# Performance work log

Measured on AMD Instinct MI355X. Metric: run time of the kernel, lower is better.

The kernel has to match this reference:

```python
import jax, jax.numpy as jnp
import numpy as np

N_EMBD = 2048
N_HEAD = 16
HEAD_DIM = N_EMBD // N_HEAD  # 128
ROPE_BASE = 10000.0


def _rope_cos_sin(T, dim, dtype):
    theta = 1.0 / (ROPE_BASE ** (jnp.arange(0, dim, 2, dtype=jnp.float32) / dim))  # [dim/2]
    freqs = jnp.arange(T, dtype=jnp.float32)[:, None] * theta[None, :]  # [T, dim/2]
    return jnp.cos(freqs).astype(dtype), jnp.sin(freqs).astype(dtype)


def _apply_rope(t, cos, sin):
    # t: [B,H,T,D]; interleaved (even, odd) pairs form complex numbers.
    B, H, T, D = t.shape
    tr = t.reshape(B, H, T, D // 2, 2)
    a, b = tr[..., 0], tr[..., 1]
    # (a + ib) * (cos + i sin)
    out = jnp.stack([a * cos - b * sin, a * sin + b * cos], axis=-1)
    return out.reshape(B, H, T, D)


def setup_inputs() -> dict:
    key = jax.random.key(0)
    k1, k2, k3 = jax.random.split(key, 3)
    B, T, C = 2, 2048, N_EMBD
    s = 1.0 / np.sqrt(C)
    return {
        "x": jax.random.normal(k1, (B, T, C), dtype=jnp.float32),
        "w_att": jax.random.normal(k2, (3 * C, C), dtype=jnp.float32) * s,
        "b_att": jnp.zeros((3 * C,), dtype=jnp.float32),
        "w_proj": jax.random.normal(k3, (C, C), dtype=jnp.float32) * s,
        "b_proj": jnp.zeros((C,), dtype=jnp.float32),
    }


def reference(x, w_att, b_att, w_proj, b_proj):
    B, T, C = x.shape
    H, D = N_HEAD, HEAD_DIM
    qkv = x @ w_att.T + b_att  # [B,T,3C]
    q, k, v = jnp.split(qkv, 3, axis=-1)
    # [B,T,C] -> [B,H,T,D]
    q, k, v = (t.reshape(B, T, H, D).transpose(0, 2, 1, 3) for t in (q, k, v))
    cos, sin = _rope_cos_sin(T, D, jnp.float32)  # [T, D/2]
    cos = cos[None, None]  # [1,1,T,D/2]
    sin = sin[None, None]
    q = _apply_rope(q, cos, sin)
    k = _apply_rope(k, cos, sin)
    # causal SDPA
    scale = 1.0 / np.sqrt(D)
    scores = jnp.einsum('bhqd,bhkd->bhqk', q, k) * scale
    mask = jnp.tril(jnp.ones((T, T), dtype=bool))
    scores = jnp.where(mask, scores, jnp.finfo(scores.dtype).min)
    attn = jax.nn.softmax(scores, axis=-1)
    y = jnp.einsum('bhqk,bhkd->bhqd', attn, v)  # [B,H,T,D]
    y = y.transpose(0, 2, 1, 3).reshape(B, T, C)
    return y @ w_proj.T + b_proj
```

## Files before the change

kernel.cpp:

```cpp
#include <hip/hip_runtime.h>
#include <hip/hip_bf16.h>
#include <math.h>

#define DEVI __device__ __forceinline__

typedef __attribute__((ext_vector_type(8))) short bf16x8;
typedef __attribute__((ext_vector_type(4))) float f32x4;

constexpr int Bn = 2;
constexpr int Tn = 2048;
constexpr int Cn = 2048;
constexpr int Hn = 16;
constexpr int Dn = 128;
constexpr int Mrows = Bn * Tn;
constexpr int Nqkv = 3 * Cn;
constexpr int BH = Bn * Hn;
constexpr int NKT = Cn / 32;

DEVI f32x4 mfma16x16(bf16x8 a, bf16x8 b, f32x4 c) {
    return __builtin_amdgcn_mfma_f32_16x16x32_bf16(a, b, c, 0, 0, 0);
}

DEVI bf16x8 load8(const __hip_bfloat16* p) {
    return *(const bf16x8*)p;
}

DEVI short bf16bits(float f) {
    union { __hip_bfloat16 b; short s; } u;
    u.b = __float2bfloat16(f);
    return u.s;
}

typedef const __attribute__((address_space(1))) void* gas1_t;
typedef __attribute__((address_space(3))) void* las3_t;
DEVI void stage16(const __hip_bfloat16* g, __hip_bfloat16* l) {
    __builtin_amdgcn_global_load_lds((gas1_t)g, (las3_t)l, 16, 0, 0);
}

DEVI bf16x8 lds8(const short* tile, int byte_off) {
    return *(const bf16x8*)((const char*)tile + byte_off);
}

__global__ __launch_bounds__(256) void cvt_kernel(
    const float* __restrict__ src, __hip_bfloat16* __restrict__ dst)
{
    const size_t i8 = ((size_t)blockIdx.x * 256 + threadIdx.x) * 8;
    const float4 a = *(const float4*)(src + i8);
    const float4 b = *(const float4*)(src + i8 + 4);
    union { bf16x8 v; __hip_bfloat16 h[8]; } u;
    u.h[0] = __float2bfloat16(a.x); u.h[1] = __float2bfloat16(a.y);
    u.h[2] = __float2bfloat16(a.z); u.h[3] = __float2bfloat16(a.w);
    u.h[4] = __float2bfloat16(b.x); u.h[5] = __float2bfloat16(b.y);
    u.h[6] = __float2bfloat16(b.z); u.h[7] = __float2bfloat16(b.w);
    *(bf16x8*)(dst + i8) = u.v;
}

__global__ __launch_bounds__(256) void qkv_gemm_kernel(
    const __hip_bfloat16* __restrict__ xb,
    const __hip_bfloat16* __restrict__ wab,
    const float* __restrict__ bias,
    __hip_bfloat16* __restrict__ Qo,
    __hip_bfloat16* __restrict__ Ko,
    __hip_bfloat16* __restrict__ Vt)
{
    __shared__ __align__(16) __hip_bfloat16 As[2][128 * 32];
    __shared__ __align__(16) __hip_bfloat16 Bs[2][128 * 32];
    const int tid  = threadIdx.x;
    const int lane = tid & 63;
    const int wid  = tid >> 6;
    const int quad = lane >> 4;
    const int l16  = lane & 15;
    const int bm = blockIdx.y * 128;
    const int bn = blockIdx.x * 128;
    const int wm = (wid >> 1) * 64;
    const int wn = (wid & 1) * 64;

    const int lr = lane >> 2;
    const int lc = (lane & 3) * 8;
    const int r0 = 32 * wid;
    const __hip_bfloat16* Ag0 = xb  + (size_t)(bm + r0 + lr) * Cn + lc;
    const __hip_bfloat16* Ag1 = xb  + (size_t)(bm + r0 + 16 + lr) * Cn + lc;
    const __hip_bfloat16* Bg0 = wab + (size_t)(bn + r0 + lr) * Cn + lc;
    const __hip_bfloat16* Bg1 = wab + (size_t)(bn + r0 + 16 + lr) * Cn + lc;
    const int lbase0 = r0 * 32 + lane * 8;
    const int lbase1 = (r0 + 16) * 32 + lane * 8;

    const f32x4 zero = {0.f, 0.f, 0.f, 0.f};
    f32x4 acc[4][4];
#pragma unroll
    for (int i = 0; i < 4; ++i)
#pragma unroll
        for (int j = 0; j < 4; ++j) acc[i][j] = zero;

    stage16(Ag0, &As[0][lbase0]);
    stage16(Ag1, &As[0][lbase1]);
    stage16(Bg0, &Bs[0][lbase0]);
    stage16(Bg1, &Bs[0][lbase1]);
    __syncthreads();

    for (int kt = 0; kt < NKT; ++kt) {
        const int cur = kt & 1;
        if (kt + 1 < NKT) {
            const int kn = (kt + 1) * 32;
            stage16(Ag0 + kn, &As[cur ^ 1][lbase0]);
            stage16(Ag1 + kn, &As[cur ^ 1][lbase1]);
            stage16(Bg0 + kn, &Bs[cur ^ 1][lbase0]);
            stage16(Bg1 + kn, &Bs[cur ^ 1][lbase1]);
        }
        bf16x8 af[4], bfr[4];
#pragma unroll
        for (int i = 0; i < 4; ++i)
            af[i] = load8(&As[cur][(wm + i * 16 + l16) * 32 + quad * 8]);
#pragma unroll
        for (int j = 0; j < 4; ++j)
            bfr[j] = load8(&Bs[cur][(wn + j * 16 + l16) * 32 + quad * 8]);
#pragma unroll
        for (int i = 0; i < 4; ++i)
#pragma unroll
            for (int j = 0; j < 4; ++j)
                acc[i][j] = mfma16x16(af[i], bfr[j], acc[i][j]);
        __syncthreads();
    }

#pragma unroll
    for (int j = 0; j < 4; ++j) {
        const int n = bn + wn + j * 16 + l16;
        const float bv = bias[n];
        const int sel = n >> 11;
        const int c   = n & 2047;
        const int h   = c >> 7;
        const int d   = c & 127;
#pragma unroll
        for (int i = 0; i < 4; ++i) {
#pragma unroll
            for (int r = 0; r < 4; ++r) {
                const int m = bm + wm + i * 16 + quad * 4 + r;
                const int b = m >> 11;
                const int t = m & 2047;
                const int bh = b * Hn + h;
                const __hip_bfloat16 hv = __float2bfloat16(acc[i][j][r] + bv);
                if (sel == 0)      Qo[((size_t)bh * Tn + t) * Dn + d] = hv;
                else if (sel == 1) Ko[((size_t)bh * Tn + t) * Dn + d] = hv;
                else               Vt[((size_t)bh * Dn + d) * Tn + t] = hv;
            }
        }
    }
}

__global__ __launch_bounds__(256) void rope_kernel(
    __hip_bfloat16* __restrict__ Qo,
    __hip_bfloat16* __restrict__ Ko)
{
    const size_t idx = (size_t)blockIdx.x * blockDim.x + threadIdx.x;
    const int d2 = (int)(idx & 63);
    const int t  = (int)((idx >> 6) & (size_t)(Tn - 1));
    const float inv = exp2f(-(float)d2 * (1.0f / 64.0f) * 13.287712379549449f);
    float sn, cs;
    sincosf((float)t * inv, &sn, &cs);
    const size_t base = (idx >> 6) * (size_t)Dn + (size_t)(2 * d2);
    {
        const float a = __bfloat162float(Qo[base]);
        const float b = __bfloat162float(Qo[base + 1]);
        Qo[base]     = __float2bfloat16(a * cs - b * sn);
        Qo[base + 1] = __float2bfloat16(a * sn + b * cs);
    }
    {
        const float a = __bfloat162float(Ko[base]);
        const float b = __bfloat162float(Ko[base + 1]);
        Ko[base]     = __float2bfloat16(a * cs - b * sn);
        Ko[base + 1] = __float2bfloat16(a * sn + b * cs);
    }
}

__global__ __launch_bounds__(256) void flash_kernel(
    const __hip_bfloat16* __restrict__ Qo,
    const __hip_bfloat16* __restrict__ Ko,
    const __hip_bfloat16* __restrict__ Vt,
    __hip_bfloat16* __restrict__ Y)
{
    __shared__ __align__(16) short Ks[2][32 * 128];
    __shared__ __align__(16) short Vs[2][128 * 32];
    __shared__ __align__(16) short Ps[4][16 * 40];
    const int tid  = threadIdx.x;
    const int lane = tid & 63;
    const int wid  = tid >> 6;
    const int quad = lane >> 4;
    const int l16  = lane & 15;
    const int bh   = blockIdx.x & (BH - 1);
    const int qblk = 31 - (blockIdx.x >> 5);
    const int q0w  = qblk * 64 + wid * 16;
    const int nkt  = 2 * qblk + 2;

    const __hip_bfloat16* Qb = Qo + (size_t)bh * Tn * Dn;
    const __hip_bfloat16* Kg = Ko + (size_t)bh * Tn * Dn;
    const __hip_bfloat16* Vg = Vt + (size_t)bh * Dn * Tn;
    short* P = &Ps[wid][0];

    const int kr = tid >> 4;
    const int ksl = (tid & 15) ^ kr;
    const __hip_bfloat16* KgA = Kg + (size_t)kr * Dn + ksl * 8;
    const int vr = tid >> 2;
    const int vsl = (tid & 3) ^ ((vr >> 1) & 3);
    const __hip_bfloat16* VgA = Vg + (size_t)vr * Tn + vsl * 8;

    int koff[4];
#pragma unroll
    for (int ks = 0; ks < 4; ++ks)
        koff[ks] = l16 * 256 + ((((ks * 4 + quad) ^ l16) & 15) << 4);
    const int vkey = ((quad ^ ((l16 >> 1) & 3)) << 4);

    bf16x8 qf[4];
#pragma unroll
    for (int ks = 0; ks < 4; ++ks)
        qf[ks] = load8(Qb + (size_t)(q0w + l16) * Dn + ks * 32 + quad * 8);

    const f32x4 zero = {0.f, 0.f, 0.f, 0.f};
    f32x4 o[8];
#pragma unroll
    for (int j = 0; j < 8; ++j) o[j] = zero;
    float lpart[4] = {0.f, 0.f, 0.f, 0.f};
    const float scale2 = 0.12751743430267602f;

    stage16(KgA,            (__hip_bfloat16*)&Ks[0][tid * 8]);
    stage16(KgA + 16 * Dn,  (__hip_bfloat16*)&Ks[0][2048 + tid * 8]);
    stage16(VgA,            (__hip_bfloat16*)&Vs[0][tid * 8]);
    stage16(VgA + 64 * Tn,  (__hip_bfloat16*)&Vs[0][2048 + tid * 8]);
    __syncthreads();

    for (int kt = 0; kt < nkt; ++kt) {
        const int cur = kt & 1;
        if (kt + 1 < nkt) {
            const int kb2 = (kt + 1) * 32;
            const int nxt = cur ^ 1;
            stage16(KgA + (size_t)kb2 * Dn,           (__hip_bfloat16*)&Ks[nxt][tid * 8]);
            stage16(KgA + (size_t)(kb2 + 16) * Dn,    (__hip_bfloat16*)&Ks[nxt][2048 + tid * 8]);
            stage16(VgA + kb2,                        (__hip_bfloat16*)&Vs[nxt][tid * 8]);
            stage16(VgA + 64 * Tn + kb2,              (__hip_bfloat16*)&Vs[nxt][2048 + tid * 8]);
        }
        const int kb = kt * 32;
        if (kb <= q0w + 15) {
            f32x4 sc0 = zero, sc1 = zero;
#pragma unroll
            for (int ks = 0; ks < 4; ++ks) {
                bf16x8 kf0 = lds8(&Ks[cur][0], koff[ks]);
                bf16x8 kf1 = lds8(&Ks[cur][0], koff[ks] + 4096);
                sc0 = mfma16x16(qf[ks], kf0, sc0);
                sc1 = mfma16x16(qf[ks], kf1, sc1);
            }
            if (kb + 31 <= q0w) {
#pragma unroll
                for (int r = 0; r < 4; ++r) {
                    const float p0 = exp2f(sc0[r] * scale2);
                    const float p1 = exp2f(sc1[r] * scale2);
                    lpart[r] += p0 + p1;
                    P[(quad * 4 + r) * 40 + l16]      = bf16bits(p0);
                    P[(quad * 4 + r) * 40 + 16 + l16] = bf16bits(p1);
                }
            } else {
#pragma unroll
                for (int r = 0; r < 4; ++r) {
                    const int row = q0w + quad * 4 + r;
                    const float a0 = (kb + l16      <= row) ? sc0[r] * scale2 : -INFINITY;
                    const float a1 = (kb + 16 + l16 <= row) ? sc1[r] * scale2 : -INFINITY;
                    const float p0 = exp2f(a0);
                    const float p1 = exp2f(a1);
                    lpart[r] += p0 + p1;
                    P[(quad * 4 + r) * 40 + l16]      = bf16bits(p0);
                    P[(quad * 4 + r) * 40 + 16 + l16] = bf16bits(p1);
                }
            }
            __builtin_amdgcn_sched_barrier(0);
            const bf16x8 af = *(const bf16x8*)(P + l16 * 40 + quad * 8);
#pragma unroll
            for (int j = 0; j < 8; ++j) {
                bf16x8 vf = lds8(&Vs[cur][0], (j * 16 + l16) * 64 + vkey);
                o[j] = mfma16x16(af, vf, o[j]);
            }
            __builtin_amdgcn_sched_barrier(0);
        }
        __syncthreads();
    }

    float invl[4];
#pragma unroll
    for (int r = 0; r < 4; ++r) {
        float s = lpart[r];
#pragma unroll
        for (int off = 1; off < 16; off <<= 1)
            s += __shfl_xor(s, off, 16);
        invl[r] = 1.0f / s;
    }

    const int b = bh >> 4;
    const int h = bh & 15;
#pragma unroll
    for (int j = 0; j < 8; ++j) {
#pragma unroll
        for (int r = 0; r < 4; ++r) {
            const int t = q0w + quad * 4 + r;
            Y[((size_t)b * Tn + t) * Cn + h * Dn + j * 16 + l16] =
                __float2bfloat16(o[j][r] * invl[r]);
        }
    }
}

__global__ __launch_bounds__(256) void proj_gemm_kernel(
    const __hip_bfloat16* __restrict__ Yb,
    const __hip_bfloat16* __restrict__ wpb,
    const float* __restrict__ bias,
    float* __restrict__ out)
{
    __shared__ __align__(16) __hip_bfloat16 As[2][128 * 32];
    __shared__ __align__(16) __hip_bfloat16 Bs[2][128 * 32];
    const int tid  = threadIdx.x;
    const int lane = tid & 63;
    const int wid  = tid >> 6;
    const int quad = lane >> 4;
    const int l16  = lane & 15;
    const int bm = blockIdx.y * 128;
    const int bn = blockIdx.x * 128;
    const int wm = (wid >> 1) * 64;
    const int wn = (wid & 1) * 64;

    const int lr = lane >> 2;
    const int lc = (lane & 3) * 8;
    const int r0 = 32 * wid;
    const __hip_bfloat16* Ag0 = Yb  + (size_t)(bm + r0 + lr) * Cn + lc;
    const __hip_bfloat16* Ag1 = Yb  + (size_t)(bm + r0 + 16 + lr) * Cn + lc;
    const __hip_bfloat16* Bg0 = wpb + (size_t)(bn + r0 + lr) * Cn + lc;
    const __hip_bfloat16* Bg1 = wpb + (size_t)(bn + r0 + 16 + lr) * Cn + lc;
    const int lbase0 = r0 * 32 + lane * 8;
    const int lbase1 = (r0 + 16) * 32 + lane * 8;

    const f32x4 zero = {0.f, 0.f, 0.f, 0.f};
    f32x4 acc[4][4];
#pragma unroll
    for (int i = 0; i < 4; ++i)
#pragma unroll
        for (int j = 0; j < 4; ++j) acc[i][j] = zero;

    stage16(Ag0, &As[0][lbase0]);
    stage16(Ag1, &As[0][lbase1]);
    stage16(Bg0, &Bs[0][lbase0]);
    stage16(Bg1, &Bs[0][lbase1]);
    __syncthreads();

    for (int kt = 0; kt < NKT; ++kt) {
        const int cur = kt & 1;
        if (kt + 1 < NKT) {
            const int kn = (kt + 1) * 32;
            stage16(Ag0 + kn, &As[cur ^ 1][lbase0]);
            stage16(Ag1 + kn, &As[cur ^ 1][lbase1]);
            stage16(Bg0 + kn, &Bs[cur ^ 1][lbase0]);
            stage16(Bg1 + kn, &Bs[cur ^ 1][lbase1]);
        }
        bf16x8 af[4], bfr[4];
#pragma unroll
        for (int i = 0; i < 4; ++i)
            af[i] = load8(&As[cur][(wm + i * 16 + l16) * 32 + quad * 8]);
#pragma unroll
        for (int j = 0; j < 4; ++j)
            bfr[j] = load8(&Bs[cur][(wn + j * 16 + l16) * 32 + quad * 8]);
#pragma unroll
        for (int i = 0; i < 4; ++i)
#pragma unroll
            for (int j = 0; j < 4; ++j)
                acc[i][j] = mfma16x16(af[i], bfr[j], acc[i][j]);
        __syncthreads();
    }

#pragma unroll
    for (int j = 0; j < 4; ++j) {
        const int n = bn + wn + j * 16 + l16;
        const float bv = bias[n];
#pragma unroll
        for (int i = 0; i < 4; ++i) {
#pragma unroll
            for (int r = 0; r < 4; ++r) {
                const int m = bm + wm + i * 16 + quad * 4 + r;
                out[(size_t)m * Cn + n] = acc[i][j][r] + bv;
            }
        }
    }
}

extern "C" void kernel_launch(void* const* d_in, const int* in_sizes, int n_in,
                              void* d_out, int out_size, void* d_ws, size_t ws_size,
                              hipStream_t stream)
{
    const float* x      = (const float*)d_in[0];
    const float* w_att  = (const float*)d_in[1];
    const float* b_att  = (const float*)d_in[2];
    const float* w_proj = (const float*)d_in[3];
    const float* b_proj = (const float*)d_in[4];
    float* out = (float*)d_out;

    const size_t per  = (size_t)BH * Tn * Dn;
    const size_t wabN = (size_t)Nqkv * Cn;
    __hip_bfloat16* Qo  = (__hip_bfloat16*)d_ws;
    __hip_bfloat16* Ko  = Qo + per;
    __hip_bfloat16* Vt  = Ko + per;
    __hip_bfloat16* xb  = Vt + per;
    __hip_bfloat16* wab = xb + per;
    __hip_bfloat16* wpb = wab + wabN;
    __hip_bfloat16* Yb  = xb;

    dim3 blk(256);
    cvt_kernel<<<dim3((Mrows * Cn) / 2048), blk, 0, stream>>>(x, xb);
    cvt_kernel<<<dim3((Nqkv * Cn) / 2048), blk, 0, stream>>>(w_att, wab);
    cvt_kernel<<<dim3((Cn * Cn) / 2048), blk, 0, stream>>>(w_proj, wpb);
    qkv_gemm_kernel<<<dim3(Nqkv / 128, Mrows / 128), blk, 0, stream>>>(
        xb, wab, b_att, Qo, Ko, Vt);
    rope_kernel<<<dim3((BH * Tn * 64) / 256), blk, 0, stream>>>(Qo, Ko);
    flash_kernel<<<dim3((Tn / 64) * BH), blk, 0, stream>>>(Qo, Ko, Vt, Yb);
    proj_gemm_kernel<<<dim3(Cn / 128, Mrows / 128), blk, 0, stream>>>(
        Yb, wpb, b_proj, out);
}
```

Measured before the change: 432.9 us.

## Rewrite QKV GEMM with 256x256 tiles, 8 waves and staged LDS pipeline

The QKV projection GEMM moves from 128x128 tiles with 4 waves and K=32 steps to 256x256 tiles with 8 waves, K=64 steps, XOR-swizzled LDS layout and a fine-grained schedule that interleaves half-tile global->LDS loads with MFMA bursts, using explicit barriers, waitcnt and setprio. It also remaps block IDs across XCDs for L2 locality. The goal is higher arithmetic intensity and better overlap of memory and matrix ops, at the cost of more registers (launch bounds 512,2), larger LDS, and fragile manual synchronisation.

```diff
diff --git a/kernel.cpp b/kernel.cpp
--- a/kernel.cpp
+++ b/kernel.cpp
@@ -16,6 +16,7 @@
 constexpr int Nqkv = 3 * Cn;
 constexpr int BH = Bn * Hn;
 constexpr int NKT = Cn / 32;
+constexpr int NKT64 = Cn / 64;
 
 DEVI f32x4 mfma16x16(bf16x8 a, bf16x8 b, f32x4 c) {
     return __builtin_amdgcn_mfma_f32_16x16x32_bf16(a, b, c, 0, 0, 0);
@@ -23,6 +24,10 @@
 
 DEVI bf16x8 load8(const __hip_bfloat16* p) {
     return *(const bf16x8*)p;
+}
+
+DEVI bf16x8 lds8c(const char* p, int byte_off) {
+    return *(const bf16x8*)(p + byte_off);
 }
 
 DEVI short bf16bits(float f) {
@@ -37,9 +42,9 @@
     __builtin_amdgcn_global_load_lds((gas1_t)g, (las3_t)l, 16, 0, 0);
 }
 
-DEVI bf16x8 lds8(const short* tile, int byte_off) {
-    return *(const bf16x8*)((const char*)tile + byte_off);
-}
+#define SBAR()  __builtin_amdgcn_s_barrier()
+#define LGKM0() do { asm volatile("s_waitcnt lgkmcnt(0)" ::: "memory"); \
+                     __builtin_amdgcn_sched_barrier(0); } while (0)
 
 __global__ __launch_bounds__(256) void cvt_kernel(
     const float* __restrict__ src, __hip_bfloat16* __restrict__ dst)
@@ -55,7 +60,110 @@
     *(bf16x8*)(dst + i8) = u.v;
 }
 
-__global__ __launch_bounds__(256) void qkv_gemm_kernel(
+template<int C>
+DEVI void qkv_tile(int t,
+    short (&Sa)[2][2][8192], short (&Sb)[2][2][8192],
+    const char* Ab, const char* Bb,
+    const __hip_bfloat16* Asrc, const __hip_bfloat16* Bsrc,
+    int sdst, f32x4 (&acc)[8][4])
+{
+    bf16x8 aA[4][2], aB[4][2], bA[2][2], bB[2][2];
+#pragma unroll
+    for (int m = 0; m < 4; ++m) {
+        aA[m][0] = lds8c(Ab, m * 2048);
+        aA[m][1] = lds8c(Ab, m * 2048 + 64);
+    }
+#pragma unroll
+    for (int j = 0; j < 2; ++j) {
+        bA[j][0] = lds8c(Bb, j * 2048);
+        bA[j][1] = lds8c(Bb, j * 2048 + 64);
+    }
+    if (t + 1 < NKT64) {
+        const __hip_bfloat16* s = Bsrc + (t + 1) * 64;
+        stage16(s,           (__hip_bfloat16*)&Sb[C ^ 1][0][sdst]);
+        stage16(s + 64 * Cn, (__hip_bfloat16*)&Sb[C ^ 1][0][4096 + sdst]);
+    }
+    SBAR();
+    LGKM0();
+    __builtin_amdgcn_s_setprio(1);
+#pragma unroll
+    for (int kk = 0; kk < 2; ++kk)
+#pragma unroll
+        for (int j = 0; j < 2; ++j)
+#pragma unroll
+            for (int m = 0; m < 4; ++m)
+                acc[m][j] = mfma16x16(aA[m][kk], bA[j][kk], acc[m][j]);
+    __builtin_amdgcn_s_setprio(0);
+    SBAR();
+#pragma unroll
+    for (int m = 0; m < 4; ++m) {
+        aB[m][0] = lds8c(Ab, 8192 + m * 2048);
+        aB[m][1] = lds8c(Ab, 8192 + m * 2048 + 64);
+    }
+    if (t + 1 < NKT64) {
+        const __hip_bfloat16* s = Bsrc + 128 * Cn + (t + 1) * 64;
+        stage16(s,           (__hip_bfloat16*)&Sb[C ^ 1][1][sdst]);
+        stage16(s + 64 * Cn, (__hip_bfloat16*)&Sb[C ^ 1][1][4096 + sdst]);
+    }
+    SBAR();
+    LGKM0();
+    __builtin_amdgcn_s_setprio(1);
+#pragma unroll
+    for (int kk = 0; kk < 2; ++kk)
+#pragma unroll
+        for (int j = 0; j < 2; ++j)
+#pragma unroll
+            for (int m = 0; m < 4; ++m)
+                acc[4 + m][j] = mfma16x16(aB[m][kk], bA[j][kk], acc[4 + m][j]);
+    __builtin_amdgcn_s_setprio(0);
+    SBAR();
+#pragma unroll
+    for (int j = 0; j < 2; ++j) {
+        bB[j][0] = lds8c(Bb, 4096 + j * 2048);
+        bB[j][1] = lds8c(Bb, 4096 + j * 2048 + 64);
+    }
+    if (t + 2 < NKT64) {
+        const __hip_bfloat16* s = Asrc + (t + 2) * 64;
+        stage16(s,           (__hip_bfloat16*)&Sa[C][0][sdst]);
+        stage16(s + 64 * Cn, (__hip_bfloat16*)&Sa[C][0][4096 + sdst]);
+    }
+    SBAR();
+    LGKM0();
+    __builtin_amdgcn_s_setprio(1);
+#pragma unroll
+    for (int kk = 0; kk < 2; ++kk)
+#pragma unroll
+        for (int j = 0; j < 2; ++j)
+#pragma unroll
+            for (int m = 0; m < 4; ++m)
+                acc[m][2 + j] = mfma16x16(aA[m][kk], bB[j][kk], acc[m][2 + j]);
+    __builtin_amdgcn_s_setprio(0);
+    SBAR();
+    if (t + 2 < NKT64) {
+        const __hip_bfloat16* s = Asrc + 128 * Cn + (t + 2) * 64;
+        stage16(s,           (__hip_bfloat16*)&Sa[C][1][sdst]);
+        stage16(s + 64 * Cn, (__hip_bfloat16*)&Sa[C][1][4096 + sdst]);
+    }
+    SBAR();
+    __builtin_amdgcn_sched_barrier(0);
+    __builtin_amdgcn_s_setprio(1);
+#pragma unroll
+    for (int kk = 0; kk < 2; ++kk)
+#pragma unroll
+        for (int j = 0; j < 2; ++j)
+#pragma unroll
+            for (int m = 0; m < 4; ++m)
+                acc[4 + m][2 + j] = mfma16x16(aB[m][kk], bB[j][kk], acc[4 + m][2 + j]);
+    __builtin_amdgcn_s_setprio(0);
+    if (t + 2 < NKT64) {
+        asm volatile("s_waitcnt vmcnt(4)" ::: "memory");
+    } else {
+        asm volatile("s_waitcnt vmcnt(0)" ::: "memory");
+    }
+    SBAR();
+}
+
+__global__ __launch_bounds__(512, 2) void qkv_gemm_kernel(
     const __hip_bfloat16* __restrict__ xb,
     const __hip_bfloat16* __restrict__ wab,
     const float* __restrict__ bias,
@@ -63,78 +171,72 @@
     __hip_bfloat16* __restrict__ Ko,
     __hip_bfloat16* __restrict__ Vt)
 {
-    __shared__ __align__(16) __hip_bfloat16 As[2][128 * 32];
-    __shared__ __align__(16) __hip_bfloat16 Bs[2][128 * 32];
+    __shared__ __align__(16) short As_[2][2][8192];
+    __shared__ __align__(16) short Bs_[2][2][8192];
     const int tid  = threadIdx.x;
     const int lane = tid & 63;
     const int wid  = tid >> 6;
     const int quad = lane >> 4;
     const int l16  = lane & 15;
-    const int bm = blockIdx.y * 128;
-    const int bn = blockIdx.x * 128;
-    const int wm = (wid >> 1) * 64;
-    const int wn = (wid & 1) * 64;
-
-    const int lr = lane >> 2;
-    const int lc = (lane & 3) * 8;
-    const int r0 = 32 * wid;
-    const __hip_bfloat16* Ag0 = xb  + (size_t)(bm + r0 + lr) * Cn + lc;
-    const __hip_bfloat16* Ag1 = xb  + (size_t)(bm + r0 + 16 + lr) * Cn + lc;
-    const __hip_bfloat16* Bg0 = wab + (size_t)(bn + r0 + lr) * Cn + lc;
-    const __hip_bfloat16* Bg1 = wab + (size_t)(bn + r0 + 16 + lr) * Cn + lc;
-    const int lbase0 = r0 * 32 + lane * 8;
-    const int lbase1 = (r0 + 16) * 32 + lane * 8;
+
+    const int wg = (blockIdx.x & 7) * 48 + (blockIdx.x >> 3);
+    const int bm = (wg / 24) * 256;
+    const int bn = (wg % 24) * 256;
+    const int wr = wid >> 2;
+    const int wc = wid & 3;
+
+    const int srow = tid >> 3;
+    const int scol = ((tid & 7) * 8) ^ (((tid >> 5) & 1) << 4);
+    const __hip_bfloat16* Asrc = xb  + (size_t)(bm + srow) * Cn + scol;
+    const __hip_bfloat16* Bsrc = wab + (size_t)(bn + srow) * Cn + scol;
+    const int sdst = tid * 8;
+
+    const int qk = (quad * 16) ^ (((l16 >> 2) & 1) << 5);
+    const char* Ab0 = (const char*)&As_[0][wr][0] + l16 * 128 + qk;
+    const char* Ab1 = (const char*)&As_[1][wr][0] + l16 * 128 + qk;
+    const char* Bb0 = (const char*)&Bs_[0][wc >> 1][0] + ((wc & 1) * 64 + l16) * 128 + qk;
+    const char* Bb1 = (const char*)&Bs_[1][wc >> 1][0] + ((wc & 1) * 64 + l16) * 128 + qk;
 
     const f32x4 zero = {0.f, 0.f, 0.f, 0.f};
-    f32x4 acc[4][4];
-#pragma unroll
-    for (int i = 0; i < 4; ++i)
+    f32x4 acc[8][4];
+#pragma unroll
+    for (int i = 0; i < 8; ++i)
 #pragma unroll
         for (int j = 0; j < 4; ++j) acc[i][j] = zero;
 
-    stage16(Ag0, &As[0][lbase0]);
-    stage16(Ag1, &As[0][lbase1]);
-    stage16(Bg0, &Bs[0][lbase0]);
-    stage16(Bg1, &Bs[0][lbase1]);
-    __syncthreads();
-
-    for (int kt = 0; kt < NKT; ++kt) {
-        const int cur = kt & 1;
-        if (kt + 1 < NKT) {
-            const int kn = (kt + 1) * 32;
-            stage16(Ag0 + kn, &As[cur ^ 1][lbase0]);
-            stage16(Ag1 + kn, &As[cur ^ 1][lbase1]);
-            stage16(Bg0 + kn, &Bs[cur ^ 1][lbase0]);
-            stage16(Bg1 + kn, &Bs[cur ^ 1][lbase1]);
-        }
-        bf16x8 af[4], bfr[4];
-#pragma unroll
-        for (int i = 0; i < 4; ++i)
-            af[i] = load8(&As[cur][(wm + i * 16 + l16) * 32 + quad * 8]);
-#pragma unroll
-        for (int j = 0; j < 4; ++j)
-            bfr[j] = load8(&Bs[cur][(wn + j * 16 + l16) * 32 + quad * 8]);
-#pragma unroll
-        for (int i = 0; i < 4; ++i)
-#pragma unroll
-            for (int j = 0; j < 4; ++j)
-                acc[i][j] = mfma16x16(af[i], bfr[j], acc[i][j]);
-        __syncthreads();
+    stage16(Asrc,                (__hip_bfloat16*)&As_[0][0][sdst]);
+    stage16(Asrc + 64 * Cn,      (__hip_bfloat16*)&As_[0][0][4096 + sdst]);
+    stage16(Asrc + 128 * Cn,     (__hip_bfloat16*)&As_[0][1][sdst]);
+    stage16(Asrc + 192 * Cn,     (__hip_bfloat16*)&As_[0][1][4096 + sdst]);
+    stage16(Bsrc,                (__hip_bfloat16*)&Bs_[0][0][sdst]);
+    stage16(Bsrc + 64 * Cn,      (__hip_bfloat16*)&Bs_[0][0][4096 + sdst]);
+    stage16(Bsrc + 128 * Cn,     (__hip_bfloat16*)&Bs_[0][1][sdst]);
+    stage16(Bsrc + 192 * Cn,     (__hip_bfloat16*)&Bs_[0][1][4096 + sdst]);
+    stage16(Asrc + 64,           (__hip_bfloat16*)&As_[1][0][sdst]);
+    stage16(Asrc + 64 * Cn + 64, (__hip_bfloat16*)&As_[1][0][4096 + sdst]);
+    stage16(Asrc + 128 * Cn + 64,(__hip_bfloat16*)&As_[1][1][sdst]);
+    stage16(Asrc + 192 * Cn + 64,(__hip_bfloat16*)&As_[1][1][4096 + sdst]);
+    asm volatile("s_waitcnt vmcnt(4)" ::: "memory");
+    SBAR();
+
+    for (int kt = 0; kt < NKT64; kt += 2) {
+        qkv_tile<0>(kt,     As_, Bs_, Ab0, Bb0, Asrc, Bsrc, sdst, acc);
+        qkv_tile<1>(kt + 1, As_, Bs_, Ab1, Bb1, Asrc, Bsrc, sdst, acc);
     }
 
 #pragma unroll
     for (int j = 0; j < 4; ++j) {
-        const int n = bn + wn + j * 16 + l16;
+        const int n = bn + wc * 64 + j * 16 + l16;
         const float bv = bias[n];
         const int sel = n >> 11;
         const int c   = n & 2047;
         const int h   = c >> 7;
         const int d   = c & 127;
 #pragma unroll
-        for (int i = 0; i < 4; ++i) {
+        for (int i = 0; i < 8; ++i) {
 #pragma unroll
             for (int r = 0; r < 4; ++r) {
-                const int m = bm + wm + i * 16 + quad * 4 + r;
+                const int m = bm + wr * 128 + i * 16 + quad * 4 + r;
                 const int b = m >> 11;
                 const int t = m & 2047;
                 const int bh = b * Hn + h;
@@ -232,18 +334,18 @@
         if (kt + 1 < nkt) {
             const int kb2 = (kt + 1) * 32;
             const int nxt = cur ^ 1;
-            stage16(KgA + (size_t)kb2 * Dn,           (__hip_bfloat16*)&Ks[nxt][tid * 8]);
-            stage16(KgA + (size_t)(kb2 + 16) * Dn,    (__hip_bfloat16*)&Ks[nxt][2048 + tid * 8]);
-            stage16(VgA + kb2,                        (__hip_bfloat16*)&Vs[nxt][tid * 8]);
-            stage16(VgA + 64 * Tn + kb2,              (__hip_bfloat16*)&Vs[nxt][2048 + tid * 8]);
+            stage16(KgA + (size_t)kb2 * Dn,        (__hip_bfloat16*)&Ks[nxt][tid * 8]);
+            stage16(KgA + (size_t)(kb2 + 16) * Dn, (__hip_bfloat16*)&Ks[nxt][2048 + tid * 8]);
+            stage16(VgA + kb2,                     (__hip_bfloat16*)&Vs[nxt][tid * 8]);
+            stage16(VgA + 64 * Tn + kb2,           (__hip_bfloat16*)&Vs[nxt][2048 + tid * 8]);
         }
         const int kb = kt * 32;
         if (kb <= q0w + 15) {
             f32x4 sc0 = zero, sc1 = zero;
 #pragma unroll
             for (int ks = 0; ks < 4; ++ks) {
-                bf16x8 kf0 = lds8(&Ks[cur][0], koff[ks]);
-                bf16x8 kf1 = lds8(&Ks[cur][0], koff[ks] + 4096);
+                bf16x8 kf0 = lds8c((const char*)&Ks[cur][0], koff[ks]);
+                bf16x8 kf1 = lds8c((const char*)&Ks[cur][0], koff[ks] + 4096);
                 sc0 = mfma16x16(qf[ks], kf0, sc0);
                 sc1 = mfma16x16(qf[ks], kf1, sc1);
             }
@@ -273,7 +375,7 @@
             const bf16x8 af = *(const bf16x8*)(P + l16 * 40 + quad * 8);
 #pragma unroll
             for (int j = 0; j < 8; ++j) {
-                bf16x8 vf = lds8(&Vs[cur][0], (j * 16 + l16) * 64 + vkey);
+                bf16x8 vf = lds8c((const char*)&Vs[cur][0], (j * 16 + l16) * 64 + vkey);
                 o[j] = mfma16x16(af, vf, o[j]);
             }
             __builtin_amdgcn_sched_barrier(0);
@@ -409,7 +511,7 @@
     cvt_kernel<<<dim3((Mrows * Cn) / 2048), blk, 0, stream>>>(x, xb);
     cvt_kernel<<<dim3((Nqkv * Cn) / 2048), blk, 0, stream>>>(w_att, wab);
     cvt_kernel<<<dim3((Cn * Cn) / 2048), blk, 0, stream>>>(w_proj, wpb);
-    qkv_gemm_kernel<<<dim3(Nqkv / 128, Mrows / 128), blk, 0, stream>>>(
+    qkv_gemm_kernel<<<dim3((Mrows / 256) * (Nqkv / 256)), dim3(512), 0, stream>>>(
         xb, wab, b_att, Qo, Ko, Vt);
     rope_kernel<<<dim3((BH * Tn * 64) / 256), blk, 0, stream>>>(Qo, Ko);
     flash_kernel<<<dim3((Tn / 64) * BH), blk, 0, stream>>>(Qo, Ko, Vt, Yb);
```

New measurement: 454.9 us. 1.05x slower.
